# Kernel tuning notes

Hardware: AMD Instinct MI355X
Metric: run time of the kernel (lower is better)

The kernel has to match this reference:

```python
import jax, jax.numpy as jnp
import numpy as np

B, S, E, H = 2, 2048, 1024, 16
D = E // H  # head_dim = 64
NEG = -1e10


def setup_inputs() -> dict:
    key = jax.random.key(0)
    ks = jax.random.split(key, 12)
    sc = 1.0 / np.sqrt(E)
    return {
        "query": jax.random.normal(ks[0], (B, S, E), jnp.float32),
        "key_": jax.random.normal(ks[1], (B, S, E), jnp.float32),
        "value": jax.random.normal(ks[2], (B, S, E), jnp.float32),
        "mask": jax.random.randint(ks[3], (B, S), 0, 2, jnp.int32),
        "Wq": jax.random.normal(ks[4], (E, E), jnp.float32) * sc,
        "bq": jnp.zeros((E,), jnp.float32),
        "Wk": jax.random.normal(ks[5], (E, E), jnp.float32) * sc,
        "bk": jnp.zeros((E,), jnp.float32),
        "Wv": jax.random.normal(ks[6], (E, E), jnp.float32) * sc,
        "bv": jnp.zeros((E,), jnp.float32),
        "Wo": jax.random.normal(ks[7], (E, E), jnp.float32) * sc,
        "bo": jnp.zeros((E,), jnp.float32),
    }


def reference(query, key_, value, mask, Wq, bq, Wk, bk, Wv, bv, Wo, bo):
    # Linear projections (torch Linear: x @ W^T + b)
    Q = (query @ Wq.T + bq).reshape(B, S, H, D)
    K = (key_ @ Wk.T + bk).reshape(B, S, H, D)
    V = (value @ Wv.T + bv).reshape(B, S, H, D)
    # [B, H, Sq, Sk] scores
    scores = jnp.einsum("bqhd,bkhd->bhqk", Q, K) / jnp.sqrt(jnp.float32(D))
    # Original sets rows of masked query positions AND columns of masked key
    # positions to -1e10 (set, not add; overlapping assignment is same value).
    pad = (mask == 0)  # [B, S]
    bad = pad[:, :, None] | pad[:, None, :]  # [B, Sq, Sk]
    scores = scores + jnp.where(bad, NEG, 0.0)[:, None, :, :]
    weights = jax.nn.softmax(scores, axis=-1)
    out = jnp.einsum("bhqk,bkhd->bqhd", weights, V).reshape(B, S, E)
    return out @ Wo.T + bo
```

## Files before the change

### kernel.cpp

```cpp
#include <hip/hip_runtime.h>

typedef __attribute__((ext_vector_type(4)))  float          f32x4;
typedef __attribute__((ext_vector_type(16))) float          f32x16;
typedef __attribute__((ext_vector_type(8)))  short          s16x8;
typedef __attribute__((ext_vector_type(4)))  unsigned short u16x4;
typedef __attribute__((ext_vector_type(8)))  unsigned short u16x8;

#define MFMA_BF16(a, b, c) __builtin_amdgcn_mfma_f32_16x16x32_bf16((a), (b), (c), 0, 0, 0)
#define MFMA32(a, b, c)    __builtin_amdgcn_mfma_f32_32x32x16_bf16((a), (b), (c), 0, 0, 0)

static constexpr int Bb = 2, Ss = 2048, Ee = 1024, Hh = 16, Dd = 64;
static constexpr size_t M4 = 4u * 1024 * 1024;
static constexpr size_t M1 = 1024 * 1024;

__device__ __forceinline__ unsigned short f2b(float f) {
    unsigned u = __builtin_bit_cast(unsigned, f);
    u += 0x7fffu + ((u >> 16) & 1u);
    return (unsigned short)(u >> 16);
}

__device__ __forceinline__ void gld_lds16(const unsigned short* g, unsigned short* l) {
    __builtin_amdgcn_global_load_lds(
        (const __attribute__((address_space(1))) unsigned int*)g,
        (__attribute__((address_space(3))) unsigned int*)l, 16, 0, 0);
}

struct CvtArgs { const float* src[7]; unsigned short* dst;
                 const int* mask; float* maskf; };

__global__ __launch_bounds__(256) void cvt_bf16(CvtArgs a)
{
    if (blockIdx.x == 8192) {
#pragma unroll
        for (int j = 0; j < 16; j++) {
            int idx = threadIdx.x + j * 256;
            a.maskf[idx] = a.mask[idx] ? 1.f : 0.f;
        }
        return;
    }
    size_t i = ((size_t)blockIdx.x * 256 + threadIdx.x) * 8;
    int seg; size_t off;
    if (i < 3 * M4) { seg = (int)(i / M4);     off = i % M4; }
    else            { size_t j = i - 3 * M4;
                      seg = 3 + (int)(j / M1); off = j % M1; }
    const float* s = a.src[seg] + off;
    f32x4 x0 = *(const f32x4*)s;
    f32x4 x1 = *(const f32x4*)(s + 4);
    u16x8 o = (u16x8){f2b(x0[0]), f2b(x0[1]), f2b(x0[2]), f2b(x0[3]),
                      f2b(x1[0]), f2b(x1[1]), f2b(x1[2]), f2b(x1[3])};
    *(u16x8*)(a.dst + i) = o;
}

template <int OUT_MODE>
__device__ __forceinline__ void gemm_bf16_body(const unsigned short* __restrict__ A,
                                               const unsigned short* __restrict__ W,
                                               const float* __restrict__ bias,
                                               void* __restrict__ Cv,
                                               int m0, int n0)
{
    __shared__ __align__(16) unsigned short Al[128 * 32];
    __shared__ __align__(16) unsigned short Bl[128 * 32];

    const int tid  = threadIdx.x;
    const int lane = tid & 63;
    const int wid  = tid >> 6;
    const int quad = lane >> 4;
    const int lr   = lane & 15;
    const int wr   = (wid >> 1) * 64;
    const int wc   = (wid & 1) * 64;

    const int srow = wid * 32 + (lane >> 2);
    const int sk8  = (lane & 3) * 8;
    const unsigned short* gA = A + (size_t)(m0 + srow) * 1024 + sk8;
    const unsigned short* gW = W + (size_t)(n0 + srow) * 1024 + sk8;
    unsigned short* lA = &Al[wid * 1024];
    unsigned short* lW = &Bl[wid * 1024];

    f32x4 acc[4][4];
#pragma unroll
    for (int i = 0; i < 4; i++)
#pragma unroll
        for (int j = 0; j < 4; j++) acc[i][j] = (f32x4){0.f, 0.f, 0.f, 0.f};

    for (int ks = 0; ks < 1024; ks += 32) {
        __syncthreads();
        gld_lds16(gA + ks,              lA);
        gld_lds16(gA + ks + 16 * 1024,  lA + 512);
        gld_lds16(gW + ks,              lW);
        gld_lds16(gW + ks + 16 * 1024,  lW + 512);
        __syncthreads();

        s16x8 af[4], bf[4];
#pragma unroll
        for (int t = 0; t < 4; t++) {
            af[t] = *(const s16x8*)&Al[(wr + t * 16 + lr) * 32 + quad * 8];
            bf[t] = *(const s16x8*)&Bl[(wc + t * 16 + lr) * 32 + quad * 8];
        }
#pragma unroll
        for (int mt = 0; mt < 4; mt++)
#pragma unroll
            for (int nt = 0; nt < 4; nt++)
                acc[mt][nt] = MFMA_BF16(af[mt], bf[nt], acc[mt][nt]);
    }

#pragma unroll
    for (int mt = 0; mt < 4; mt++)
#pragma unroll
        for (int nt = 0; nt < 4; nt++) {
            int   col  = n0 + wc + nt * 16 + lr;
            float bcol = bias[col];
            int   rbase = m0 + wr + mt * 16 + quad * 4;
            if (OUT_MODE == 2) {
                int bb = rbase >> 11, s = rbase & 2047;
                u16x4 pk;
#pragma unroll
                for (int r = 0; r < 4; r++) pk[r] = f2b(acc[mt][nt][r] + bcol);
                *(u16x4*)&((unsigned short*)Cv)[((size_t)(bb * 1024 + col)) * 2048 + s] = pk;
            } else {
#pragma unroll
                for (int r = 0; r < 4; r++) {
                    float v = acc[mt][nt][r] + bcol;
                    if (OUT_MODE == 3) v *= 0.180336884f;
                    ((unsigned short*)Cv)[(size_t)(rbase + r) * 1024 + col] = f2b(v);
                }
            }
        }
}

struct GArgs {
    const unsigned short* A[3];
    const unsigned short* W[3];
    const float* bias[3];
    unsigned short* C[3];
};

__global__ __launch_bounds__(256) void proj_gemm(GArgs ga)
{
    const int id  = blockIdx.x;
    const int xcd = id & 7;
    const int t   = id >> 3;
    const int z   = t >> 5;
    const int tt  = t & 31;
    const int n0  = (tt & 7) * 128;
    const int m0  = (xcd * 4 + (tt >> 3)) * 128;

    if (z == 2)      gemm_bf16_body<2>(ga.A[2], ga.W[2], ga.bias[2], ga.C[2], m0, n0);
    else if (z == 1) gemm_bf16_body<1>(ga.A[1], ga.W[1], ga.bias[1], ga.C[1], m0, n0);
    else             gemm_bf16_body<3>(ga.A[0], ga.W[0], ga.bias[0], ga.C[0], m0, n0);
}

__global__ __launch_bounds__(256)
void out_gemm(const unsigned short* __restrict__ A,
              const unsigned short* __restrict__ W,
              const float* __restrict__ bias,
              float* __restrict__ C)
{
    __shared__ __align__(16) unsigned short Al[128 * 32];
    __shared__ __align__(16) unsigned short Bl[64 * 32];

    const int id  = blockIdx.x;
    const int xcd = id & 7;
    const int t   = id >> 3;
    const int n0  = (t & 15) * 64;
    const int m0  = (xcd * 4 + (t >> 4)) * 128;

    const int tid  = threadIdx.x;
    const int lane = tid & 63;
    const int wid  = tid >> 6;
    const int quad = lane >> 4;
    const int lr   = lane & 15;
    const int wr   = (wid >> 1) * 64;
    const int wc   = (wid & 1) * 32;

    const int srowA = wid * 32 + (lane >> 2);
    const int srowW = wid * 16 + (lane >> 2);
    const int sk8   = (lane & 3) * 8;
    const unsigned short* gA = A + (size_t)(m0 + srowA) * 1024 + sk8;
    const unsigned short* gW = W + (size_t)(n0 + srowW) * 1024 + sk8;
    unsigned short* lA = &Al[wid * 1024];
    unsigned short* lW = &Bl[wid * 512];

    f32x4 acc[4][2];
#pragma unroll
    for (int i = 0; i < 4; i++)
#pragma unroll
        for (int j = 0; j < 2; j++) acc[i][j] = (f32x4){0.f, 0.f, 0.f, 0.f};

    for (int ks = 0; ks < 1024; ks += 32) {
        __syncthreads();
        gld_lds16(gA + ks,              lA);
        gld_lds16(gA + ks + 16 * 1024,  lA + 512);
        gld_lds16(gW + ks,              lW);
        __syncthreads();

        s16x8 af[4], bf[2];
#pragma unroll
        for (int mt = 0; mt < 4; mt++)
            af[mt] = *(const s16x8*)&Al[(wr + mt * 16 + lr) * 32 + quad * 8];
#pragma unroll
        for (int nt = 0; nt < 2; nt++)
            bf[nt] = *(const s16x8*)&Bl[(wc + nt * 16 + lr) * 32 + quad * 8];
#pragma unroll
        for (int mt = 0; mt < 4; mt++)
#pragma unroll
            for (int nt = 0; nt < 2; nt++)
                acc[mt][nt] = MFMA_BF16(af[mt], bf[nt], acc[mt][nt]);
    }

#pragma unroll
    for (int mt = 0; mt < 4; mt++)
#pragma unroll
        for (int nt = 0; nt < 2; nt++) {
            int   col  = n0 + wc + nt * 16 + lr;
            float bcol = bias[col];
            int   rbase = m0 + wr + mt * 16 + quad * 4;
#pragma unroll
            for (int r = 0; r < 4; r++)
                C[(size_t)(rbase + r) * 1024 + col] = acc[mt][nt][r] + bcol;
        }
}

__global__ __launch_bounds__(256)
void flash_attn(const unsigned short* __restrict__ Q,
                const unsigned short* __restrict__ K,
                const unsigned short* __restrict__ Vt,
                const float* __restrict__ maskf,
                unsigned short* __restrict__ O)
{
    constexpr int   ST  = 76;
    constexpr float EPS = 9.31322575e-10f;
    __shared__ __align__(16) unsigned short Kl[64 * ST];
    __shared__ __align__(16) unsigned short Vl[64 * ST];
    __shared__ __align__(16) unsigned short Pl[64 * ST];
    __shared__ float lsq[4][32];

    const int id    = blockIdx.x;
    const int xcd   = id & 7;
    const int local = id >> 3;
    const int pair  = xcd * 4 + (local >> 5);
    const int b     = pair >> 4;
    const int h     = pair & 15;
    const int q0    = (local & 31) * 64;

    const int tid  = threadIdx.x;
    const int lane = tid & 63;
    const int wid  = tid >> 6;
    const int l31  = lane & 31;
    const int hl   = lane >> 5;
    const int qh   = wid & 1;
    const int kh   = wid >> 1;

    const unsigned short* qg =
        Q + (size_t)(b * 2048 + q0 + qh * 32 + l31) * 1024 + h * 64 + hl * 8;
    s16x8 qf[4];
#pragma unroll
    for (int db = 0; db < 4; db++) qf[db] = *(const s16x8*)(qg + db * 16);

    const float  mq  = maskf[b * 2048 + q0 + qh * 32 + l31];
    const float* mkp = maskf + b * 2048;

    const int lk = (tid >> 3) * ST + (tid & 7) * 8;
    const unsigned short* gK = K  + (size_t)(b * 2048 + (tid >> 3)) * 1024 + h * 64 + (tid & 7) * 8;
    const unsigned short* gV = Vt + (size_t)(b * 1024 + h * 64 + (tid >> 3)) * 2048 + (tid & 7) * 8;

    float  lsum = 0.f;
    f32x16 accO = (f32x16){0.f,0.f,0.f,0.f,0.f,0.f,0.f,0.f,
                           0.f,0.f,0.f,0.f,0.f,0.f,0.f,0.f};

    for (int kt = 0; kt < 2048; kt += 64) {
        __syncthreads();
        *(u16x8*)&Kl[lk]           = *(const u16x8*)(gK + (size_t)kt * 1024);
        *(u16x8*)&Kl[lk + 32 * ST] = *(const u16x8*)(gK + (size_t)(kt + 32) * 1024);
        *(u16x8*)&Vl[lk]           = *(const u16x8*)(gV + kt);
        *(u16x8*)&Vl[lk + 32 * ST] = *(const u16x8*)(gV + kt + (size_t)32 * 2048);
        __syncthreads();

        f32x16 st = (f32x16){0.f,0.f,0.f,0.f,0.f,0.f,0.f,0.f,
                             0.f,0.f,0.f,0.f,0.f,0.f,0.f,0.f};
#pragma unroll
        for (int db = 0; db < 4; db++) {
            s16x8 kf = *(const s16x8*)&Kl[(kh * 32 + l31) * ST + db * 16 + hl * 8];
            st = MFMA32(kf, qf[db], st);
        }
#pragma unroll
        for (int rq = 0; rq < 4; rq++) {
            int   kb = 4 * hl + 8 * rq;
            f32x4 m4 = *(const f32x4*)&mkp[kt + kh * 32 + kb];
            unsigned u[4];
#pragma unroll
            for (int r = 0; r < 4; r++) {
                float e = __builtin_amdgcn_exp2f(st[rq * 4 + r]);
                float p = e * (m4[r] * mq) + EPS;
                lsum += p;
                u[r] = __builtin_bit_cast(unsigned, p) + 0x8000u;
            }
            uint2 w;
            w.x = __builtin_amdgcn_perm(u[1], u[0], 0x07060302u);
            w.y = __builtin_amdgcn_perm(u[3], u[2], 0x07060302u);
            *(uint2*)&Pl[(qh * 32 + l31) * ST + kh * 32 + kb] = w;
        }
        __syncthreads();

#pragma unroll
        for (int ks = 0; ks < 4; ks++) {
            s16x8 pf = *(const s16x8*)&Pl[(qh * 32 + l31) * ST + ks * 16 + hl * 8];
            s16x8 vf = *(const s16x8*)&Vl[(kh * 32 + l31) * ST + ks * 16 + hl * 8];
            accO = MFMA32(pf, vf, accO);
        }
    }

    lsum += __shfl_xor(lsum, 32, 64);
    lsq[wid][l31] = lsum;
    __syncthreads();

#pragma unroll
    for (int rq = 0; rq < 4; rq++) {
        int   qr = 4 * hl + 8 * rq;
        f32x4 lA = *(const f32x4*)&lsq[qh][qr];
        f32x4 lB = *(const f32x4*)&lsq[qh + 2][qr];
#pragma unroll
        for (int r = 0; r < 4; r++) {
            float val = accO[rq * 4 + r] * __builtin_amdgcn_rcpf(lA[r] + lB[r]);
            O[(size_t)(b * 2048 + q0 + qh * 32 + qr + r) * 1024 + h * 64 +
              kh * 32 + l31] = f2b(val);
        }
    }
}

extern "C" void kernel_launch(void* const* d_in, const int* in_sizes, int n_in,
                              void* d_out, int out_size, void* d_ws, size_t ws_size,
                              hipStream_t stream)
{
    const float* query = (const float*)d_in[0];
    const float* key_  = (const float*)d_in[1];
    const float* value = (const float*)d_in[2];
    const int*   mask  = (const int*)d_in[3];
    const float* Wq    = (const float*)d_in[4];
    const float* bq    = (const float*)d_in[5];
    const float* Wk    = (const float*)d_in[6];
    const float* bk    = (const float*)d_in[7];
    const float* Wv    = (const float*)d_in[8];
    const float* bv    = (const float*)d_in[9];
    const float* Wo    = (const float*)d_in[10];
    const float* bo    = (const float*)d_in[11];
    float* out = (float*)d_out;

    unsigned short* cvt = (unsigned short*)d_ws;
    unsigned short* Aq  = cvt;
    unsigned short* Ak  = cvt + M4;
    unsigned short* Av  = cvt + 2 * M4;
    unsigned short* Wqb = cvt + 3 * M4;
    unsigned short* Wkb = Wqb + M1;
    unsigned short* Wvb = Wkb + M1;
    unsigned short* Wob = Wvb + M1;
    unsigned short* Qb  = Wob + M1;
    unsigned short* Kb  = Qb + M4;
    unsigned short* Vt  = Kb + M4;
    unsigned short* Ab  = Vt + M4;
    float*          mkf = (float*)(Ab + M4);

    CvtArgs ca;
    ca.src[0] = query; ca.src[1] = key_; ca.src[2] = value;
    ca.src[3] = Wq; ca.src[4] = Wk; ca.src[5] = Wv; ca.src[6] = Wo;
    ca.dst = cvt; ca.mask = mask; ca.maskf = mkf;
    cvt_bf16<<<dim3(8193), 256, 0, stream>>>(ca);

    GArgs ga;
    ga.A[0] = Aq;  ga.A[1] = Ak;  ga.A[2] = Av;
    ga.W[0] = Wqb; ga.W[1] = Wkb; ga.W[2] = Wvb;
    ga.bias[0] = bq; ga.bias[1] = bk; ga.bias[2] = bv;
    ga.C[0] = Qb; ga.C[1] = Kb; ga.C[2] = Vt;
    proj_gemm<<<dim3(768), 256, 0, stream>>>(ga);

    flash_attn<<<dim3(1024), 256, 0, stream>>>(Qb, Kb, Vt, mkf, Ab);
    out_gemm<<<dim3(512), 256, 0, stream>>>(Ab, Wob, bo, out);
}
```

Measured before the change: 234.7 us.

## Double-buffer LDS tiles in projection and output GEMMs to overlap loads

Measured after the change: 268.1 us. +14.2%, slower.

```diff
diff --git a/kernel.cpp b/kernel.cpp
--- a/kernel.cpp
+++ b/kernel.cpp
@@ -58,8 +58,8 @@
                                                void* __restrict__ Cv,
                                                int m0, int n0)
 {
-    __shared__ __align__(16) unsigned short Al[128 * 32];
-    __shared__ __align__(16) unsigned short Bl[128 * 32];
+    __shared__ __align__(16) unsigned short Al[2][128 * 32];
+    __shared__ __align__(16) unsigned short Bl[2][128 * 32];
 
     const int tid  = threadIdx.x;
     const int lane = tid & 63;
@@ -73,8 +73,7 @@
     const int sk8  = (lane & 3) * 8;
     const unsigned short* gA = A + (size_t)(m0 + srow) * 1024 + sk8;
     const unsigned short* gW = W + (size_t)(n0 + srow) * 1024 + sk8;
-    unsigned short* lA = &Al[wid * 1024];
-    unsigned short* lW = &Bl[wid * 1024];
+    const int swid = wid * 1024;
 
     f32x4 acc[4][4];
 #pragma unroll
@@ -82,25 +81,37 @@
 #pragma unroll
         for (int j = 0; j < 4; j++) acc[i][j] = (f32x4){0.f, 0.f, 0.f, 0.f};
 
-    for (int ks = 0; ks < 1024; ks += 32) {
-        __syncthreads();
-        gld_lds16(gA + ks,              lA);
-        gld_lds16(gA + ks + 16 * 1024,  lA + 512);
-        gld_lds16(gW + ks,              lW);
-        gld_lds16(gW + ks + 16 * 1024,  lW + 512);
-        __syncthreads();
+    gld_lds16(gA,             &Al[0][swid]);
+    gld_lds16(gA + 16 * 1024, &Al[0][swid + 512]);
+    gld_lds16(gW,             &Bl[0][swid]);
+    gld_lds16(gW + 16 * 1024, &Bl[0][swid + 512]);
+    __syncthreads();
+
+#pragma unroll 2
+    for (int it = 0; it < 32; ++it) {
+        const int cur = it & 1;
+        if (it + 1 < 32) {
+            const int ks  = (it + 1) * 32;
+            const int nxt = cur ^ 1;
+            gld_lds16(gA + ks,             &Al[nxt][swid]);
+            gld_lds16(gA + ks + 16 * 1024, &Al[nxt][swid + 512]);
+            gld_lds16(gW + ks,             &Bl[nxt][swid]);
+            gld_lds16(gW + ks + 16 * 1024, &Bl[nxt][swid + 512]);
+        }
 
         s16x8 af[4], bf[4];
 #pragma unroll
         for (int t = 0; t < 4; t++) {
-            af[t] = *(const s16x8*)&Al[(wr + t * 16 + lr) * 32 + quad * 8];
-            bf[t] = *(const s16x8*)&Bl[(wc + t * 16 + lr) * 32 + quad * 8];
+            af[t] = *(const s16x8*)&Al[cur][(wr + t * 16 + lr) * 32 + quad * 8];
+            bf[t] = *(const s16x8*)&Bl[cur][(wc + t * 16 + lr) * 32 + quad * 8];
         }
 #pragma unroll
         for (int mt = 0; mt < 4; mt++)
 #pragma unroll
             for (int nt = 0; nt < 4; nt++)
                 acc[mt][nt] = MFMA_BF16(af[mt], bf[nt], acc[mt][nt]);
+
+        __syncthreads();
     }
 
 #pragma unroll
@@ -155,8 +166,8 @@
               const float* __restrict__ bias,
               float* __restrict__ C)
 {
-    __shared__ __align__(16) unsigned short Al[128 * 32];
-    __shared__ __align__(16) unsigned short Bl[64 * 32];
+    __shared__ __align__(16) unsigned short Al[2][128 * 32];
+    __shared__ __align__(16) unsigned short Bl[2][64 * 32];
 
     const int id  = blockIdx.x;
     const int xcd = id & 7;
@@ -177,8 +188,8 @@
     const int sk8   = (lane & 3) * 8;
     const unsigned short* gA = A + (size_t)(m0 + srowA) * 1024 + sk8;
     const unsigned short* gW = W + (size_t)(n0 + srowW) * 1024 + sk8;
-    unsigned short* lA = &Al[wid * 1024];
-    unsigned short* lW = &Bl[wid * 512];
+    const int swidA = wid * 1024;
+    const int swidW = wid * 512;
 
     f32x4 acc[4][2];
 #pragma unroll
@@ -186,25 +197,36 @@
 #pragma unroll
         for (int j = 0; j < 2; j++) acc[i][j] = (f32x4){0.f, 0.f, 0.f, 0.f};
 
-    for (int ks = 0; ks < 1024; ks += 32) {
-        __syncthreads();
-        gld_lds16(gA + ks,              lA);
-        gld_lds16(gA + ks + 16 * 1024,  lA + 512);
-        gld_lds16(gW + ks,              lW);
-        __syncthreads();
+    gld_lds16(gA,             &Al[0][swidA]);
+    gld_lds16(gA + 16 * 1024, &Al[0][swidA + 512]);
+    gld_lds16(gW,             &Bl[0][swidW]);
+    __syncthreads();
+
+#pragma unroll 2
+    for (int it = 0; it < 32; ++it) {
+        const int cur = it & 1;
+        if (it + 1 < 32) {
+            const int ks  = (it + 1) * 32;
+            const int nxt = cur ^ 1;
+            gld_lds16(gA + ks,             &Al[nxt][swidA]);
+            gld_lds16(gA + ks + 16 * 1024, &Al[nxt][swidA + 512]);
+            gld_lds16(gW + ks,             &Bl[nxt][swidW]);
+        }
 
         s16x8 af[4], bf[2];
 #pragma unroll
         for (int mt = 0; mt < 4; mt++)
-            af[mt] = *(const s16x8*)&Al[(wr + mt * 16 + lr) * 32 + quad * 8];
+            af[mt] = *(const s16x8*)&Al[cur][(wr + mt * 16 + lr) * 32 + quad * 8];
 #pragma unroll
         for (int nt = 0; nt < 2; nt++)
-            bf[nt] = *(const s16x8*)&Bl[(wc + nt * 16 + lr) * 32 + quad * 8];
+            bf[nt] = *(const s16x8*)&Bl[cur][(wc + nt * 16 + lr) * 32 + quad * 8];
 #pragma unroll
         for (int mt = 0; mt < 4; mt++)
 #pragma unroll
             for (int nt = 0; nt < 2; nt++)
                 acc[mt][nt] = MFMA_BF16(af[mt], bf[nt], acc[mt][nt]);
+
+        __syncthreads();
     }
 
 #pragma unroll
```

## Keep P in registers via lane shuffles, split-K PV with end reduction

Applied to the files above, without the earlier changes.

Result: slower. 336.9 us (+43.5%).

```diff
diff --git a/kernel.cpp b/kernel.cpp
--- a/kernel.cpp
+++ b/kernel.cpp
@@ -5,6 +5,7 @@
 typedef __attribute__((ext_vector_type(8)))  short          s16x8;
 typedef __attribute__((ext_vector_type(4)))  unsigned short u16x4;
 typedef __attribute__((ext_vector_type(8)))  unsigned short u16x8;
+typedef __attribute__((ext_vector_type(4)))  unsigned int   u32x4;
 
 #define MFMA_BF16(a, b, c) __builtin_amdgcn_mfma_f32_16x16x32_bf16((a), (b), (c), 0, 0, 0)
 #define MFMA32(a, b, c)    __builtin_amdgcn_mfma_f32_32x32x16_bf16((a), (b), (c), 0, 0, 0)
@@ -229,10 +230,10 @@
 {
     constexpr int   ST  = 76;
     constexpr float EPS = 9.31322575e-10f;
-    __shared__ __align__(16) unsigned short Kl[64 * ST];
-    __shared__ __align__(16) unsigned short Vl[64 * ST];
-    __shared__ __align__(16) unsigned short Pl[64 * ST];
+    __shared__ __align__(16) unsigned char smemb[2 * 64 * ST * 2];
     __shared__ float lsq[4][32];
+    unsigned short* Kl = (unsigned short*)smemb;
+    unsigned short* Vl = (unsigned short*)(smemb + 64 * ST * 2);
 
     const int id    = blockIdx.x;
     const int xcd   = id & 7;
@@ -264,8 +265,9 @@
     const unsigned short* gV = Vt + (size_t)(b * 1024 + h * 64 + (tid >> 3)) * 2048 + (tid & 7) * 8;
 
     float  lsum = 0.f;
-    f32x16 accO = (f32x16){0.f,0.f,0.f,0.f,0.f,0.f,0.f,0.f,
-                           0.f,0.f,0.f,0.f,0.f,0.f,0.f,0.f};
+    f32x16 accO0 = (f32x16){0.f,0.f,0.f,0.f,0.f,0.f,0.f,0.f,
+                            0.f,0.f,0.f,0.f,0.f,0.f,0.f,0.f};
+    f32x16 accO1 = accO0;
 
     for (int kt = 0; kt < 2048; kt += 64) {
         __syncthreads();
@@ -282,6 +284,8 @@
             s16x8 kf = *(const s16x8*)&Kl[(kh * 32 + l31) * ST + db * 16 + hl * 8];
             st = MFMA32(kf, qf[db], st);
         }
+
+        unsigned w[4][2];
 #pragma unroll
         for (int rq = 0; rq < 4; rq++) {
             int   kb = 4 * hl + 8 * rq;
@@ -294,35 +298,68 @@
                 lsum += p;
                 u[r] = __builtin_bit_cast(unsigned, p) + 0x8000u;
             }
-            uint2 w;
-            w.x = __builtin_amdgcn_perm(u[1], u[0], 0x07060302u);
-            w.y = __builtin_amdgcn_perm(u[3], u[2], 0x07060302u);
-            *(uint2*)&Pl[(qh * 32 + l31) * ST + kh * 32 + kb] = w;
-        }
-        __syncthreads();
-
-#pragma unroll
-        for (int ks = 0; ks < 4; ks++) {
-            s16x8 pf = *(const s16x8*)&Pl[(qh * 32 + l31) * ST + ks * 16 + hl * 8];
-            s16x8 vf = *(const s16x8*)&Vl[(kh * 32 + l31) * ST + ks * 16 + hl * 8];
-            accO = MFMA32(pf, vf, accO);
-        }
+            w[rq][0] = __builtin_amdgcn_perm(u[1], u[0], 0x07060302u);
+            w[rq][1] = __builtin_amdgcn_perm(u[3], u[2], 0x07060302u);
+        }
+
+        unsigned e0 = hl ? w[0][0] : w[1][0];
+        unsigned e1 = hl ? w[0][1] : w[1][1];
+        unsigned e2 = hl ? w[2][0] : w[3][0];
+        unsigned e3 = hl ? w[2][1] : w[3][1];
+        e0 = (unsigned)__shfl_xor((int)e0, 32, 64);
+        e1 = (unsigned)__shfl_xor((int)e1, 32, 64);
+        e2 = (unsigned)__shfl_xor((int)e2, 32, 64);
+        e3 = (unsigned)__shfl_xor((int)e3, 32, 64);
+
+        u32x4 pw0 = hl ? (u32x4){e0, e1, w[1][0], w[1][1]}
+                       : (u32x4){w[0][0], w[0][1], e0, e1};
+        u32x4 pw1 = hl ? (u32x4){e2, e3, w[3][0], w[3][1]}
+                       : (u32x4){w[2][0], w[2][1], e2, e3};
+        s16x8 pf0 = __builtin_bit_cast(s16x8, pw0);
+        s16x8 pf1 = __builtin_bit_cast(s16x8, pw1);
+
+        const int cb = kh * 32 + hl * 8;
+        s16x8 v00 = *(const s16x8*)&Vl[l31 * ST + cb];
+        s16x8 v01 = *(const s16x8*)&Vl[l31 * ST + cb + 16];
+        s16x8 v10 = *(const s16x8*)&Vl[(32 + l31) * ST + cb];
+        s16x8 v11 = *(const s16x8*)&Vl[(32 + l31) * ST + cb + 16];
+        accO0 = MFMA32(pf0, v00, accO0);
+        accO0 = MFMA32(pf1, v01, accO0);
+        accO1 = MFMA32(pf0, v10, accO1);
+        accO1 = MFMA32(pf1, v11, accO1);
     }
 
     lsum += __shfl_xor(lsum, 32, 64);
     lsq[wid][l31] = lsum;
     __syncthreads();
 
-#pragma unroll
-    for (int rq = 0; rq < 4; rq++) {
-        int   qr = 4 * hl + 8 * rq;
-        f32x4 lA = *(const f32x4*)&lsq[qh][qr];
-        f32x4 lB = *(const f32x4*)&lsq[qh + 2][qr];
-#pragma unroll
-        for (int r = 0; r < 4; r++) {
-            float val = accO[rq * 4 + r] * __builtin_amdgcn_rcpf(lA[r] + lB[r]);
-            O[(size_t)(b * 2048 + q0 + qh * 32 + qr + r) * 1024 + h * 64 +
-              kh * 32 + l31] = f2b(val);
+    float* red = (float*)smemb;
+    {
+        float* rw = red + (qh * 2 + (kh ^ 1)) * 1024;
+#pragma unroll
+        for (int rq = 0; rq < 4; rq++)
+#pragma unroll
+            for (int r = 0; r < 4; r++) {
+                int row = 4 * hl + 8 * rq + r;
+                rw[row * 32 + l31] = kh ? accO0[rq * 4 + r] : accO1[rq * 4 + r];
+            }
+    }
+    __syncthreads();
+    {
+        const float* rr = red + (qh * 2 + kh) * 1024;
+#pragma unroll
+        for (int rq = 0; rq < 4; rq++) {
+            int   qr = 4 * hl + 8 * rq;
+            f32x4 lA = *(const f32x4*)&lsq[qh][qr];
+            f32x4 lB = *(const f32x4*)&lsq[qh + 2][qr];
+#pragma unroll
+            for (int r = 0; r < 4; r++) {
+                float own = kh ? accO1[rq * 4 + r] : accO0[rq * 4 + r];
+                float val = (own + rr[(qr + r) * 32 + l31]) *
+                            __builtin_amdgcn_rcpf(lA[r] + lB[r]);
+                O[(size_t)(b * 2048 + q0 + qh * 32 + qr + r) * 1024 + h * 64 +
+                  kh * 32 + l31] = f2b(val);
+            }
         }
     }
 }
```

## Software-pipeline flash attention: defer PV MFMA to next iteration with double-buffered P/V

Applied to the files above, without the earlier changes.

Result: slower. 246.9 us (+5.2%).

```diff
diff --git a/kernel.cpp b/kernel.cpp
--- a/kernel.cpp
+++ b/kernel.cpp
@@ -230,8 +230,8 @@
     constexpr int   ST  = 76;
     constexpr float EPS = 9.31322575e-10f;
     __shared__ __align__(16) unsigned short Kl[64 * ST];
-    __shared__ __align__(16) unsigned short Vl[64 * ST];
-    __shared__ __align__(16) unsigned short Pl[64 * ST];
+    __shared__ __align__(16) unsigned short Vl[2][64 * ST];
+    __shared__ __align__(16) unsigned short Pl[2][64 * ST];
     __shared__ float lsq[4][32];
 
     const int id    = blockIdx.x;
@@ -263,16 +263,38 @@
     const unsigned short* gK = K  + (size_t)(b * 2048 + (tid >> 3)) * 1024 + h * 64 + (tid & 7) * 8;
     const unsigned short* gV = Vt + (size_t)(b * 1024 + h * 64 + (tid >> 3)) * 2048 + (tid & 7) * 8;
 
+    const int prow = (qh * 32 + l31) * ST;
+    const int v0row = (kh * 32 + l31) * ST;
+
     float  lsum = 0.f;
     f32x16 accO = (f32x16){0.f,0.f,0.f,0.f,0.f,0.f,0.f,0.f,
                            0.f,0.f,0.f,0.f,0.f,0.f,0.f,0.f};
 
-    for (int kt = 0; kt < 2048; kt += 64) {
-        __syncthreads();
-        *(u16x8*)&Kl[lk]           = *(const u16x8*)(gK + (size_t)kt * 1024);
-        *(u16x8*)&Kl[lk + 32 * ST] = *(const u16x8*)(gK + (size_t)(kt + 32) * 1024);
-        *(u16x8*)&Vl[lk]           = *(const u16x8*)(gV + kt);
-        *(u16x8*)&Vl[lk + 32 * ST] = *(const u16x8*)(gV + kt + (size_t)32 * 2048);
+    for (int t = 0; t < 32; ++t) {
+        const int kt  = t * 64;
+        const int cur = t & 1;
+        const int prv = cur ^ 1;
+
+        __syncthreads();
+
+        u16x8 rk0 = *(const u16x8*)(gK + (size_t)kt * 1024);
+        u16x8 rk1 = *(const u16x8*)(gK + (size_t)(kt + 32) * 1024);
+        u16x8 rv0 = *(const u16x8*)(gV + kt);
+        u16x8 rv1 = *(const u16x8*)(gV + kt + (size_t)32 * 2048);
+
+        if (t) {
+#pragma unroll
+            for (int ks = 0; ks < 4; ks++) {
+                s16x8 pf = *(const s16x8*)&Pl[prv][prow + ks * 16 + hl * 8];
+                s16x8 vf = *(const s16x8*)&Vl[prv][v0row + ks * 16 + hl * 8];
+                accO = MFMA32(pf, vf, accO);
+            }
+        }
+
+        *(u16x8*)&Kl[lk]                = rk0;
+        *(u16x8*)&Kl[lk + 32 * ST]      = rk1;
+        *(u16x8*)&Vl[cur][lk]           = rv0;
+        *(u16x8*)&Vl[cur][lk + 32 * ST] = rv1;
         __syncthreads();
 
         f32x16 st = (f32x16){0.f,0.f,0.f,0.f,0.f,0.f,0.f,0.f,
@@ -297,21 +319,20 @@
             uint2 w;
             w.x = __builtin_amdgcn_perm(u[1], u[0], 0x07060302u);
             w.y = __builtin_amdgcn_perm(u[3], u[2], 0x07060302u);
-            *(uint2*)&Pl[(qh * 32 + l31) * ST + kh * 32 + kb] = w;
-        }
-        __syncthreads();
-
-#pragma unroll
-        for (int ks = 0; ks < 4; ks++) {
-            s16x8 pf = *(const s16x8*)&Pl[(qh * 32 + l31) * ST + ks * 16 + hl * 8];
-            s16x8 vf = *(const s16x8*)&Vl[(kh * 32 + l31) * ST + ks * 16 + hl * 8];
-            accO = MFMA32(pf, vf, accO);
+            *(uint2*)&Pl[cur][prow + kh * 32 + kb] = w;
         }
     }
 
     lsum += __shfl_xor(lsum, 32, 64);
     lsq[wid][l31] = lsum;
     __syncthreads();
+
+#pragma unroll
+    for (int ks = 0; ks < 4; ks++) {
+        s16x8 pf = *(const s16x8*)&Pl[1][prow + ks * 16 + hl * 8];
+        s16x8 vf = *(const s16x8*)&Vl[1][v0row + ks * 16 + hl * 8];
+        accO = MFMA32(pf, vf, accO);
+    }
 
 #pragma unroll
     for (int rq = 0; rq < 4; rq++) {
```
